# Kernel tuning notes

Hardware: AMD Instinct MI355X
Metric: run time of the kernel (lower is better)

## Reference

```python
import jax, jax.numpy as jnp
import numpy as np

V = 100          # atoms per molecule (reactant and every candidate product)
C = 1000         # number of candidate products (B - 1)
E_R = 250        # directed edges in reactant graph
E_P = C * E_R    # total edges over all candidate product graphs
NODE_IN = 82     # WLN atom feature size
EDGE_IN = 6      # WLN bond feature size
H = 128          # node_hidden_feats
N_LAYERS = 3     # num_encode_gnn_layers


def setup_inputs() -> dict:
    key = jax.random.key(0)
    ks = jax.random.split(key, 20)
    # reactant graph edges
    r_src = jax.random.randint(ks[0], (E_R,), 0, V)
    r_dst = jax.random.randint(ks[1], (E_R,), 0, V)
    # candidate product graphs: random edges within each graph, offset per graph
    p_src_local = jax.random.randint(ks[2], (C, E_R), 0, V)
    p_dst_local = jax.random.randint(ks[3], (C, E_R), 0, V)
    offsets = (jnp.arange(C) * V)[:, None]
    p_src = (p_src_local + offsets).reshape(-1)
    p_dst = (p_dst_local + offsets).reshape(-1)

    def rn(k, shape, scale=0.1):
        return jax.random.normal(k, shape, dtype=jnp.float32) * scale

    return dict(
        reactant_node_feats=rn(ks[4], (V, NODE_IN), 1.0),
        reactant_edge_feats=rn(ks[5], (E_R, EDGE_IN), 1.0),
        product_node_feats=rn(ks[6], (C * V, NODE_IN), 1.0),
        product_edge_feats=rn(ks[7], (E_P, EDGE_IN), 1.0),
        candidate_scores=rn(ks[8], (C, 1), 1.0),
        # shared-weight WLN encoder (used for both reactant and products)
        W_proj=rn(ks[9], (NODE_IN, H)), b_proj=jnp.zeros((H,), jnp.float32),
        W_msg=rn(ks[10], (H + EDGE_IN, H)), b_msg=jnp.zeros((H,), jnp.float32),
        W_new=rn(ks[11], (2 * H, H)), b_new=jnp.zeros((H,), jnp.float32),
        # diff WLN (1 layer, no input projection)
        W_msg_d=rn(ks[12], (H + EDGE_IN, H)), b_msg_d=jnp.zeros((H,), jnp.float32),
        W_new_d=rn(ks[13], (2 * H, H)), b_new_d=jnp.zeros((H,), jnp.float32),
        # prediction head
        W_pred1=rn(ks[14], (H, H)), b_pred1=jnp.zeros((H,), jnp.float32),
        W_pred2=rn(ks[15], (H, 1)), b_pred2=jnp.zeros((1,), jnp.float32),
        reactant_src=r_src, reactant_dst=r_dst,
        product_src=p_src, product_dst=p_dst,
    )


def _wln_layers(h, e, src, dst, n_nodes, W_msg, b_msg, W_new, b_new, n_layers):
    # dgllife WLN: message/update MLP weights are SHARED across the n_layers iterations.
    for _ in range(n_layers):
        # per-edge message: ReLU(Linear([h_src ; e]))  -- [E, H]
        m = jax.nn.relu(jnp.concatenate([h[src], e], axis=1) @ W_msg + b_msg)
        # scatter-sum messages to destination nodes -- [N, H]
        agg = jax.ops.segment_sum(m, dst, num_segments=n_nodes)
        # node update: ReLU(Linear([h ; agg]))
        h = jax.nn.relu(jnp.concatenate([h, agg], axis=1) @ W_new + b_new)
    return h


def reference(reactant_node_feats, reactant_edge_feats, product_node_feats,
              product_edge_feats, candidate_scores,
              W_proj, b_proj, W_msg, b_msg, W_new, b_new,
              W_msg_d, b_msg_d, W_new_d, b_new_d,
              W_pred1, b_pred1, W_pred2, b_pred2,
              reactant_src, reactant_dst, product_src, product_dst):
    # encoder WLN (project_in_feats=True, 3 shared-weight layers)
    r = jax.nn.relu(reactant_node_feats @ W_proj + b_proj)
    r = _wln_layers(r, reactant_edge_feats, reactant_src, reactant_dst, V,
                    W_msg, b_msg, W_new, b_new, N_LAYERS)            # [V, H]
    p = jax.nn.relu(product_node_feats @ W_proj + b_proj)
    p = _wln_layers(p, product_edge_feats, product_src, product_dst, C * V,
                    W_msg, b_msg, W_new, b_new, N_LAYERS)            # [C*V, H]
    # node-wise difference against broadcast reactant features
    diff = (p.reshape(C, V, H) - r[None, :, :]).reshape(-1, H)       # [C*V, H]
    # diff WLN (project_in_feats=False, 1 layer)
    d = _wln_layers(diff, product_edge_feats, product_src, product_dst, C * V,
                    W_msg_d, b_msg_d, W_new_d, b_new_d, 1)           # [C*V, H]
    # sum pooling per candidate graph (each graph has exactly V nodes)
    g = d.reshape(C, V, H).sum(axis=1)                               # [C, H]
    # MLP scorer + candidate scores
    return jax.nn.relu(g @ W_pred1 + b_pred1) @ W_pred2 + b_pred2 + candidate_scores
```

## Files before the change

### kernel.cpp

```cpp
#include <hip/hip_runtime.h>
#include <hip/hip_bf16.h>
#include <cstdint>

#define H 128
#define VV 100
#define CC 1000
#define ER_N 250
#define NODE_IN_N 82
#define EDGE_IN_N 6
#define LDA 136
#define NT 512
#define NP_TOT 100000

typedef short short8 __attribute__((ext_vector_type(8)));
typedef float floatx4 __attribute__((ext_vector_type(4)));
typedef __hip_bfloat16 bf16;

#define OFF_B0 0
#define OFF_B1 27200
#define OFF_EF 54400
#define OFF_RP 62400
#define OFF_CNT 62816
#define OFF_SD 63232
#define OFF_EIDX 64240
#define OFF_RED 65248
#define OFF_G 67296
#define SMEM_TOTAL 67808

#define PREP_W (27 * 4096)
#define PREP_X (NP_TOT * 48)
__global__ __launch_bounds__(256) void prep_all(
    const float* __restrict__ Wp, const float* __restrict__ Wm,
    const float* __restrict__ Wn, const float* __restrict__ Wmd,
    const float* __restrict__ Wnd, const float* __restrict__ Xp,
    const float* __restrict__ Epe,
    bf16* __restrict__ wfrag, bf16* __restrict__ Xbf, float* __restrict__ Epad) {
  long idx = (long)blockIdx.x * 256 + threadIdx.x;
  if (idx < PREP_W) {
    const float* W;
    int Ksrc;
    long local = idx;
    if (idx < 3 * 4096)       { W = Wp;  Ksrc = NODE_IN_N; }
    else if (idx < 7 * 4096)  { W = Wm;  Ksrc = H;     local -= 3 * 4096; }
    else if (idx < 15 * 4096) { W = Wn;  Ksrc = 2 * H; local -= 7 * 4096; }
    else if (idx < 19 * 4096) { W = Wmd; Ksrc = H;     local -= 15 * 4096; }
    else                      { W = Wnd; Ksrc = 2 * H; local -= 19 * 4096; }
    int j = local & 7, lane = (local >> 3) & 63, nt = (local >> 9) & 7, kc = local >> 12;
    int k = kc * 32 + ((lane >> 4) & 3) * 8 + j;
    int n = nt * 16 + (lane & 15);
    float v = (k < Ksrc) ? W[(size_t)k * H + n] : 0.f;
    wfrag[idx] = __float2bfloat16(v);
    return;
  }
  idx -= PREP_W;
  if (idx < (long)PREP_X) {
    long r = idx / 48;
    int p = (int)(idx - r * 48);
    int c0 = 2 * p;
    float v0 = (c0 < NODE_IN_N) ? Xp[r * NODE_IN_N + c0] : 0.f;
    float v1 = (c0 + 1 < NODE_IN_N) ? Xp[r * NODE_IN_N + c0 + 1] : 0.f;
    __hip_bfloat162 pk;
    pk.x = __float2bfloat16(v0);
    pk.y = __float2bfloat16(v1);
    *(__hip_bfloat162*)&Xbf[r * 96 + c0] = pk;
    return;
  }
  idx -= (long)PREP_X;
  if (idx < (long)NP_TOT * 20) {
    long e = idx >> 3;
    int k = (int)(idx & 7);
    Epad[idx] = (k < EDGE_IN_N) ? Epe[e * EDGE_IN_N + k] : 0.f;
  }
}

template<int CHUNKS>
__device__ __forceinline__ void load_bfrag(short8 b[CHUNKS], const bf16* __restrict__ Wf,
                                           int nt8, int lane) {
#pragma unroll
  for (int kc = 0; kc < CHUNKS; ++kc)
    b[kc] = *(const short8*)(Wf + ((size_t)((kc * 8 + nt8) * 64 + lane)) * 8);
}

template<int CHUNKS>
__device__ __forceinline__ void mfma_m7(floatx4 acc[7], const short8 b[CHUNKS],
                                        const bf16* A, int l16, int quad) {
#pragma unroll
  for (int kc = 0; kc < CHUNKS; ++kc)
#pragma unroll
    for (int mi = 0; mi < 7; ++mi) {
      short8 a = *(const short8*)(A + (mi * 16 + l16) * LDA + kc * 32 + quad * 8);
      acc[mi] = __builtin_amdgcn_mfma_f32_16x16x32_bf16(a, b[kc], acc[mi], 0, 0, 0);
    }
}

__device__ __forceinline__ void epi(floatx4 acc[7], const float* __restrict__ bias,
                                    bool relu, bf16* Out, int nt8, int quad, int l16) {
  int col = nt8 * 16 + l16;
  float bb = bias[col];
#pragma unroll
  for (int mi = 0; mi < 7; ++mi)
#pragma unroll
    for (int r = 0; r < 4; ++r) {
      int row = mi * 16 + quad * 4 + r;
      if (row < VV) {
        float v = acc[mi][r] + bb;
        if (relu) v = fmaxf(v, 0.f);
        Out[row * LDA + col] = __float2bfloat16(v);
      }
    }
}

__device__ __forceinline__ void zero7(floatx4 acc[7]) {
#pragma unroll
  for (int mi = 0; mi < 7; ++mi) acc[mi] = (floatx4){0.f, 0.f, 0.f, 0.f};
}

__device__ __forceinline__ void gather(const bf16* Y, bf16* X, const float* sEf,
                                       const int* sRowPtr, const int* sEidx,
                                       const float* __restrict__ WmBot,
                                       int q8, int c2) {
  float wb[EDGE_IN_N][2];
#pragma unroll
  for (int k = 0; k < EDGE_IN_N; ++k) {
    float2 w2 = *(const float2*)&WmBot[k * H + 2 * c2];
    wb[k][0] = w2.x;
    wb[k][1] = w2.y;
  }
#pragma unroll
  for (int i = 0; i < 13; ++i) {
    int n = q8 + 8 * i;
    if (n < VV) {
      int p0 = sRowPtr[n], p1 = sRowPtr[n + 1];
      float a0 = 0.f, a1 = 0.f;
      for (int p = p0; p < p1; ++p) {
        int v = sEidx[p];
        int s = v & 127, e = v >> 7;
        uint32_t tt = *(const uint32_t*)&Y[s * LDA + 2 * c2];
        float u0 = __uint_as_float((tt & 0xffffu) << 16);
        float u1 = __uint_as_float((tt >> 16) << 16);
        float4 ea = *(const float4*)&sEf[e * 8];
        float2 eb = *(const float2*)&sEf[e * 8 + 4];
        u0 = fmaf(ea.x, wb[0][0], u0); u1 = fmaf(ea.x, wb[0][1], u1);
        u0 = fmaf(ea.y, wb[1][0], u0); u1 = fmaf(ea.y, wb[1][1], u1);
        u0 = fmaf(ea.z, wb[2][0], u0); u1 = fmaf(ea.z, wb[2][1], u1);
        u0 = fmaf(ea.w, wb[3][0], u0); u1 = fmaf(ea.w, wb[3][1], u1);
        u0 = fmaf(eb.x, wb[4][0], u0); u1 = fmaf(eb.x, wb[4][1], u1);
        u0 = fmaf(eb.y, wb[5][0], u0); u1 = fmaf(eb.y, wb[5][1], u1);
        a0 += fmaxf(u0, 0.f);
        a1 += fmaxf(u1, 0.f);
      }
      __hip_bfloat162 pk;
      pk.x = __float2bfloat16(a0);
      pk.y = __float2bfloat16(a1);
      *(__hip_bfloat162*)&X[n * LDA + 2 * c2] = pk;
    }
  }
}

__device__ __forceinline__ void wln_layer(
    bf16* X, bf16* Y, const float* sEf, const int* sRowPtr, const int* sEidx,
    const bf16* __restrict__ wf_msg, const float* __restrict__ bmsg,
    const float* __restrict__ WmBot,
    const bf16* __restrict__ wf_new, const float* __restrict__ bnew,
    int lane, int nt8, int quad, int l16, int q8, int c2) {
  short8 bm_[4], bu1[4], bu2[4];
  floatx4 accM[7], accU[7];
  load_bfrag<4>(bm_, wf_msg, nt8, lane);
  zero7(accM);
  mfma_m7<4>(accM, bm_, X, l16, quad);
  load_bfrag<4>(bu1, wf_new, nt8, lane);
  epi(accM, bmsg, false, Y, nt8, quad, l16);
  __syncthreads();
  zero7(accU);
  mfma_m7<4>(accU, bu1, X, l16, quad);
  load_bfrag<4>(bu2, wf_new + 4 * 4096, nt8, lane);
  __syncthreads();
  gather(Y, X, sEf, sRowPtr, sEidx, WmBot, q8, c2);
  __syncthreads();
  mfma_m7<4>(accU, bu2, X, l16, quad);
  epi(accU, bnew, true, Y, nt8, quad, l16);
  __syncthreads();
}

template<bool PRODUCT>
__global__ __launch_bounds__(NT, 4) void wln_fused(
    const void* __restrict__ Xin, const void* __restrict__ EFin,
    const int* __restrict__ SRC, const int* __restrict__ DST,
    const bf16* __restrict__ wf_proj, const float* __restrict__ bproj,
    const bf16* __restrict__ wf_msg, const float* __restrict__ bmsg,
    const float* __restrict__ WmBot,
    const bf16* __restrict__ wf_new, const float* __restrict__ bnew,
    const bf16* __restrict__ wf_msgd, const float* __restrict__ bmsgd,
    const float* __restrict__ WmdBot,
    const bf16* __restrict__ wf_newd, const float* __restrict__ bnewd,
    bf16* __restrict__ hr_global,
    const float* __restrict__ W1, const float* __restrict__ b1,
    const float* __restrict__ W2, const float* __restrict__ b2,
    const float* __restrict__ scores, float* __restrict__ out) {
  __shared__ __align__(16) char smem[SMEM_TOTAL];
  bf16* sB0 = (bf16*)(smem + OFF_B0);
  bf16* sB1 = (bf16*)(smem + OFF_B1);
  float* sEf = (float*)(smem + OFF_EF);
  int* sRowPtr = (int*)(smem + OFF_RP);
  int* sCnt = (int*)(smem + OFF_CNT);
  int* sSD = (int*)(smem + OFF_SD);
  int* sEidx = (int*)(smem + OFF_EIDX);
  float* sRed = (float*)(smem + OFF_RED);
  float* sG = (float*)(smem + OFF_G);

  const int tid = threadIdx.x;
  const int lane = tid & 63;
  const int wave = tid >> 6;
  const int quad = (lane >> 4) & 3, l16 = lane & 15;
  const int nt8 = wave;
  const int q8 = tid >> 6, c2 = tid & 63;
  const int c = blockIdx.x;
  const int no = c * VV;
  const long eo = (long)c * ER_N;

  if (tid < VV) sCnt[tid] = 0;
  __syncthreads();
  if (tid < ER_N) {
    int s = SRC[eo + tid] - no;
    int d = DST[eo + tid] - no;
    sSD[tid] = (d << 16) | s;
    atomicAdd(&sCnt[d], 1);
  }
  if (PRODUCT) {
    const float4* Ep = (const float4*)((const float*)EFin + eo * 8);
    for (int f = tid; f < 500; f += NT) ((float4*)sEf)[f] = Ep[f];
    const bf16* Xb = (const bf16*)Xin + (size_t)no * 96;
    for (int f = tid; f < 1200; f += NT) {
      int r = f / 12, g = f - r * 12;
      *(float4*)&sB0[r * LDA + g * 8] = *(const float4*)(Xb + r * 96 + g * 8);
    }
  } else {
    const float* Ef = (const float*)EFin;
    for (int f = tid; f < ER_N * EDGE_IN_N; f += NT) {
      int e = f / EDGE_IN_N, k = f - e * EDGE_IN_N;
      sEf[e * 8 + k] = Ef[f];
    }
    const float* X = (const float*)Xin;
    for (int f = tid; f < VV * 96; f += NT) {
      int r = f / 96, cc = f - r * 96;
      float v = (cc < NODE_IN_N) ? X[r * NODE_IN_N + cc] : 0.f;
      sB0[r * LDA + cc] = __float2bfloat16(v);
    }
  }
  __syncthreads();

  if (wave == 0) {
    int c0 = sCnt[lane];
    int c1 = (lane + 64 < VV) ? sCnt[lane + 64] : 0;
    int v = c0;
#pragma unroll
    for (int d = 1; d < 64; d <<= 1) {
      int t = __shfl_up(v, d, 64);
      if (lane >= d) v += t;
    }
    int total0 = __shfl(v, 63, 64);
    int w = c1;
#pragma unroll
    for (int d = 1; d < 64; d <<= 1) {
      int t = __shfl_up(w, d, 64);
      if (lane >= d) w += t;
    }
    int ex0 = v - c0;
    int ex1 = total0 + w - c1;
    sRowPtr[lane] = ex0;
    sCnt[lane] = ex0;
    if (lane + 64 < VV) {
      sRowPtr[lane + 64] = ex1;
      sCnt[lane + 64] = ex1;
    }
    if (lane == 0) sRowPtr[VV] = ER_N;
  }
  __syncthreads();
  if (tid < ER_N) {
    int sd = sSD[tid];
    int p = atomicAdd(&sCnt[sd >> 16], 1);
    sEidx[p] = (sd & 0xffff) | (tid << 7);
  }
  __syncthreads();

  {
    short8 bp_[3];
    floatx4 acc[7];
    load_bfrag<3>(bp_, wf_proj, nt8, lane);
    zero7(acc);
    mfma_m7<3>(acc, bp_, sB0, l16, quad);
    epi(acc, bproj, true, sB1, nt8, quad, l16);
  }
  __syncthreads();

  bf16* Hb = sB1;
  bf16* Tb = sB0;

  for (int l = 0; l < 3; ++l) {
    wln_layer(Hb, Tb, sEf, sRowPtr, sEidx, wf_msg, bmsg, WmBot, wf_new, bnew,
              lane, nt8, quad, l16, q8, c2);
    bf16* tmp = Hb; Hb = Tb; Tb = tmp;
  }

  if (!PRODUCT) {
    for (int f = tid; f < VV * H; f += NT)
      hr_global[f] = Hb[(f >> 7) * LDA + (f & 127)];
    return;
  }

  for (int f = tid; f < VV * H; f += NT) {
    int r = f >> 7, j = f & 127;
    float v = __bfloat162float(Hb[r * LDA + j]) - __bfloat162float(hr_global[f]);
    Hb[r * LDA + j] = __float2bfloat16(v);
  }
  __syncthreads();

  wln_layer(Hb, Tb, sEf, sRowPtr, sEidx, wf_msgd, bmsgd, WmdBot, wf_newd, bnewd,
            lane, nt8, quad, l16, q8, c2);
  { bf16* tmp = Hb; Hb = Tb; Tb = tmp; }

  {
    int j = tid & 127, qq = tid >> 7;
    float p = 0.f;
    for (int v = qq * 25; v < qq * 25 + 25; ++v)
      p += __bfloat162float(Hb[v * LDA + j]);
    sRed[tid] = p;
  }
  __syncthreads();
  if (tid < H) {
    float s = 0.f;
#pragma unroll
    for (int q = 0; q < 4; ++q) s += sRed[q * 128 + tid];
    sG[tid] = s;
  }
  __syncthreads();
  {
    int j = tid & 127, qq = tid >> 7;
    float a = 0.f;
    for (int k = qq * 32; k < qq * 32 + 32; ++k)
      a = fmaf(sG[k], W1[(size_t)k * H + j], a);
    sRed[tid] = a;
  }
  __syncthreads();
  if (tid < H) {
    float m = b1[tid];
#pragma unroll
    for (int q = 0; q < 4; ++q) m += sRed[q * 128 + tid];
    sG[tid] = fmaxf(m, 0.f) * W2[tid];
  }
  __syncthreads();
  if (wave == 0) {
    float v = sG[lane] + sG[lane + 64];
#pragma unroll
    for (int d = 32; d > 0; d >>= 1) v += __shfl_down(v, d, 64);
    if (lane == 0) out[c] = v + b2[0] + scores[c];
  }
}

extern "C" void kernel_launch(void* const* d_in, const int* in_sizes, int n_in,
                              void* d_out, int out_size, void* d_ws, size_t ws_size,
                              hipStream_t stream) {
  const float* Xr  = (const float*)d_in[0];
  const float* Ere = (const float*)d_in[1];
  const float* Xp  = (const float*)d_in[2];
  const float* Epe = (const float*)d_in[3];
  const float* sc  = (const float*)d_in[4];
  const float* Wp  = (const float*)d_in[5];
  const float* bp  = (const float*)d_in[6];
  const float* Wm  = (const float*)d_in[7];
  const float* bm  = (const float*)d_in[8];
  const float* Wn  = (const float*)d_in[9];
  const float* bn  = (const float*)d_in[10];
  const float* Wmd = (const float*)d_in[11];
  const float* bmd = (const float*)d_in[12];
  const float* Wnd = (const float*)d_in[13];
  const float* bnd = (const float*)d_in[14];
  const float* W1  = (const float*)d_in[15];
  const float* b1  = (const float*)d_in[16];
  const float* W2  = (const float*)d_in[17];
  const float* b2  = (const float*)d_in[18];
  const int* rsrc  = (const int*)d_in[19];
  const int* rdst  = (const int*)d_in[20];
  const int* psrc  = (const int*)d_in[21];
  const int* pdst  = (const int*)d_in[22];

  bf16* wf_proj = (bf16*)d_ws;
  bf16* wf_msg  = wf_proj + 3 * 4096;
  bf16* wf_new  = wf_msg + 4 * 4096;
  bf16* wf_msgd = wf_new + 8 * 4096;
  bf16* wf_newd = wf_msgd + 4 * 4096;
  bf16* hr      = wf_newd + 8 * 4096;
  bf16* Xbf     = hr + VV * H;
  float* Epad   = (float*)(Xbf + (size_t)NP_TOT * 96);

  float* out = (float*)d_out;

  {
    long total = (long)PREP_W + (long)PREP_X + (long)NP_TOT * 20;
    int blocks = (int)((total + 255) / 256);
    prep_all<<<blocks, 256, 0, stream>>>(Wp, Wm, Wn, Wmd, Wnd, Xp, Epe,
                                         wf_proj, Xbf, Epad);
  }

  wln_fused<false><<<1, NT, 0, stream>>>(
      Xr, Ere, rsrc, rdst, wf_proj, bp, wf_msg, bm, Wm + H * H, wf_new, bn,
      wf_msgd, bmd, Wmd + H * H, wf_newd, bnd, hr, W1, b1, W2, b2, sc, out);
  wln_fused<true><<<CC, NT, 0, stream>>>(
      Xbf, Epad, psrc, pdst, wf_proj, bp, wf_msg, bm, Wm + H * H, wf_new, bn,
      wf_msgd, bmd, Wmd + H * H, wf_newd, bnd, hr, W1, b1, W2, b2, sc, out);
}
```

Baseline: 300.4 us.

## Merge reactant and product launches using a global flag handoff

Folds the single-block reactant encoder launch into the product launch as block 0. Product blocks run their three encoder layers concurrently and spin on a global release/acquire flag only before the difference step. This is meant to remove the serial launch and tail of the one-block reactant kernel. The cost is a spin-wait that depends on block 0 being scheduled, which holds in practice because it is the lowest block index, plus atomic loads of the reactant features.

```diff
diff --git a/kernel.cpp b/kernel.cpp
--- a/kernel.cpp
+++ b/kernel.cpp
@@ -34,8 +34,10 @@
     const float* __restrict__ Wn, const float* __restrict__ Wmd,
     const float* __restrict__ Wnd, const float* __restrict__ Xp,
     const float* __restrict__ Epe,
-    bf16* __restrict__ wfrag, bf16* __restrict__ Xbf, float* __restrict__ Epad) {
+    bf16* __restrict__ wfrag, bf16* __restrict__ Xbf, float* __restrict__ Epad,
+    int* __restrict__ flag) {
   long idx = (long)blockIdx.x * 256 + threadIdx.x;
+  if (idx == 0) *flag = 0;
   if (idx < PREP_W) {
     const float* W;
     int Ksrc;
@@ -182,10 +184,11 @@
   __syncthreads();
 }
 
-template<bool PRODUCT>
 __global__ __launch_bounds__(NT, 4) void wln_fused(
-    const void* __restrict__ Xin, const void* __restrict__ EFin,
-    const int* __restrict__ SRC, const int* __restrict__ DST,
+    const float* __restrict__ Xr, const float* __restrict__ Ere,
+    const int* __restrict__ rsrc, const int* __restrict__ rdst,
+    const bf16* __restrict__ Xbf, const float* __restrict__ Epad,
+    const int* __restrict__ psrc, const int* __restrict__ pdst,
     const bf16* __restrict__ wf_proj, const float* __restrict__ bproj,
     const bf16* __restrict__ wf_msg, const float* __restrict__ bmsg,
     const float* __restrict__ WmBot,
@@ -193,7 +196,7 @@
     const bf16* __restrict__ wf_msgd, const float* __restrict__ bmsgd,
     const float* __restrict__ WmdBot,
     const bf16* __restrict__ wf_newd, const float* __restrict__ bnewd,
-    bf16* __restrict__ hr_global,
+    bf16* __restrict__ hr_global, int* __restrict__ flag,
     const float* __restrict__ W1, const float* __restrict__ b1,
     const float* __restrict__ W2, const float* __restrict__ b2,
     const float* __restrict__ scores, float* __restrict__ out) {
@@ -214,36 +217,36 @@
   const int quad = (lane >> 4) & 3, l16 = lane & 15;
   const int nt8 = wave;
   const int q8 = tid >> 6, c2 = tid & 63;
-  const int c = blockIdx.x;
+  const bool REAC = (blockIdx.x == 0);
+  const int c = REAC ? 0 : (blockIdx.x - 1);
   const int no = c * VV;
   const long eo = (long)c * ER_N;
 
   if (tid < VV) sCnt[tid] = 0;
   __syncthreads();
   if (tid < ER_N) {
-    int s = SRC[eo + tid] - no;
-    int d = DST[eo + tid] - no;
+    int s, d;
+    if (REAC) { s = rsrc[tid]; d = rdst[tid]; }
+    else      { s = psrc[eo + tid] - no; d = pdst[eo + tid] - no; }
     sSD[tid] = (d << 16) | s;
     atomicAdd(&sCnt[d], 1);
   }
-  if (PRODUCT) {
-    const float4* Ep = (const float4*)((const float*)EFin + eo * 8);
+  if (!REAC) {
+    const float4* Ep = (const float4*)(Epad + eo * 8);
     for (int f = tid; f < 500; f += NT) ((float4*)sEf)[f] = Ep[f];
-    const bf16* Xb = (const bf16*)Xin + (size_t)no * 96;
+    const bf16* Xb = Xbf + (size_t)no * 96;
     for (int f = tid; f < 1200; f += NT) {
       int r = f / 12, g = f - r * 12;
       *(float4*)&sB0[r * LDA + g * 8] = *(const float4*)(Xb + r * 96 + g * 8);
     }
   } else {
-    const float* Ef = (const float*)EFin;
     for (int f = tid; f < ER_N * EDGE_IN_N; f += NT) {
       int e = f / EDGE_IN_N, k = f - e * EDGE_IN_N;
-      sEf[e * 8 + k] = Ef[f];
-    }
-    const float* X = (const float*)Xin;
+      sEf[e * 8 + k] = Ere[f];
+    }
     for (int f = tid; f < VV * 96; f += NT) {
       int r = f / 96, cc = f - r * 96;
-      float v = (cc < NODE_IN_N) ? X[r * NODE_IN_N + cc] : 0.f;
+      float v = (cc < NODE_IN_N) ? Xr[r * NODE_IN_N + cc] : 0.f;
       sB0[r * LDA + cc] = __float2bfloat16(v);
     }
   }
@@ -302,16 +305,37 @@
     bf16* tmp = Hb; Hb = Tb; Tb = tmp;
   }
 
-  if (!PRODUCT) {
-    for (int f = tid; f < VV * H; f += NT)
-      hr_global[f] = Hb[(f >> 7) * LDA + (f & 127)];
+  if (REAC) {
+    for (int f = tid; f < VV * H / 2; f += NT) {
+      int r = f >> 6, j = (f & 63) * 2;
+      uint32_t pk = *(const uint32_t*)&Hb[r * LDA + j];
+      __hip_atomic_store((uint32_t*)hr_global + f, pk,
+                         __ATOMIC_RELAXED, __HIP_MEMORY_SCOPE_AGENT);
+    }
+    __syncthreads();
+    if (tid == 0)
+      __hip_atomic_store(flag, 1, __ATOMIC_RELEASE, __HIP_MEMORY_SCOPE_AGENT);
     return;
   }
 
-  for (int f = tid; f < VV * H; f += NT) {
-    int r = f >> 7, j = f & 127;
-    float v = __bfloat162float(Hb[r * LDA + j]) - __bfloat162float(hr_global[f]);
-    Hb[r * LDA + j] = __float2bfloat16(v);
+  if (tid == 0) {
+    while (__hip_atomic_load(flag, __ATOMIC_ACQUIRE, __HIP_MEMORY_SCOPE_AGENT) == 0)
+      __builtin_amdgcn_s_sleep(16);
+  }
+  __syncthreads();
+  for (int f = tid; f < VV * H / 2; f += NT) {
+    int r = f >> 6, j = (f & 63) * 2;
+    uint32_t rk = __hip_atomic_load((const uint32_t*)hr_global + f,
+                                    __ATOMIC_RELAXED, __HIP_MEMORY_SCOPE_AGENT);
+    uint32_t hk = *(const uint32_t*)&Hb[r * LDA + j];
+    float h0 = __uint_as_float((hk & 0xffffu) << 16) -
+               __uint_as_float((rk & 0xffffu) << 16);
+    float h1 = __uint_as_float((hk >> 16) << 16) -
+               __uint_as_float((rk >> 16) << 16);
+    __hip_bfloat162 o;
+    o.x = __float2bfloat16(h0);
+    o.y = __float2bfloat16(h1);
+    *(__hip_bfloat162*)&Hb[r * LDA + j] = o;
   }
   __syncthreads();
 
@@ -392,6 +416,7 @@
   bf16* hr      = wf_newd + 8 * 4096;
   bf16* Xbf     = hr + VV * H;
   float* Epad   = (float*)(Xbf + (size_t)NP_TOT * 96);
+  int* flag     = (int*)(Epad + (size_t)250000 * 8);
 
   float* out = (float*)d_out;
 
@@ -399,13 +424,12 @@
     long total = (long)PREP_W + (long)PREP_X + (long)NP_TOT * 20;
     int blocks = (int)((total + 255) / 256);
     prep_all<<<blocks, 256, 0, stream>>>(Wp, Wm, Wn, Wmd, Wnd, Xp, Epe,
-                                         wf_proj, Xbf, Epad);
-  }
-
-  wln_fused<false><<<1, NT, 0, stream>>>(
-      Xr, Ere, rsrc, rdst, wf_proj, bp, wf_msg, bm, Wm + H * H, wf_new, bn,
-      wf_msgd, bmd, Wmd + H * H, wf_newd, bnd, hr, W1, b1, W2, b2, sc, out);
-  wln_fused<true><<<CC, NT, 0, stream>>>(
-      Xbf, Epad, psrc, pdst, wf_proj, bp, wf_msg, bm, Wm + H * H, wf_new, bn,
-      wf_msgd, bmd, Wmd + H * H, wf_newd, bnd, hr, W1, b1, W2, b2, sc, out);
-}
+                                         wf_proj, Xbf, Epad, flag);
+  }
+
+  wln_fused<<<CC + 1, NT, 0, stream>>>(
+      Xr, Ere, rsrc, rdst, Xbf, Epad, psrc, pdst,
+      wf_proj, bp, wf_msg, bm, Wm + H * H, wf_new, bn,
+      wf_msgd, bmd, Wmd + H * H, wf_newd, bnd, hr, flag,
+      W1, b1, W2, b2, sc, out);
+}
```

Result: faster. 280.7 us (-6.6%).
